# Kernel optimization log

Measured on AMD Instinct MI355X. Metric: run time of the kernel, lower is better.

The kernel has to match this reference:

```python
import jax, jax.numpy as jnp
import numpy as np

B, S, D, H, E, K = 4, 2048, 1024, 2048, 8, 2


def setup_inputs() -> dict:
    key = jax.random.key(0)
    ks = jax.random.split(key, 5)
    x = jax.random.normal(ks[0], (B, S, D), dtype=jnp.float32)
    Wr = jax.random.normal(ks[1], (D, E), dtype=jnp.float32) * 0.02  # router weight
    w1 = jax.random.normal(ks[2], (E, D, H), dtype=jnp.float32) * 0.02  # gate proj per expert
    w3 = jax.random.normal(ks[3], (E, D, H), dtype=jnp.float32) * 0.02  # up proj per expert
    w2 = jax.random.normal(ks[4], (E, H, D), dtype=jnp.float32) * 0.02  # down proj per expert
    return {"x": x, "Wr": Wr, "w1": w1, "w2": w2, "w3": w3}


def reference(x, Wr, w1, w2, w3):
    b, s, d = x.shape
    e = Wr.shape[1]
    flat = x.reshape(b * s, d)                      # [T, D]
    logits = flat @ Wr                              # [T, E]
    probs = jax.nn.softmax(logits, axis=-1)
    vals, idx = jax.lax.top_k(probs, K)             # [T, K]
    weights = vals / jnp.sum(vals, axis=-1, keepdims=True)
    onehot = jax.nn.one_hot(idx, e, dtype=flat.dtype)   # [T, K, E]
    cw = jnp.einsum('tke,tk->te', onehot, weights)      # combine weight per (token, expert)

    # naive dense: every expert computes every token, masked by combine weights
    out = jnp.zeros_like(flat)
    for ei in range(e):  # fixed small structural loop over experts
        h = jax.nn.silu(flat @ w1[ei]) * (flat @ w3[ei])   # [T, H]
        out = out + (h @ w2[ei]) * cw[:, ei:ei + 1]

    # aux load-balancing loss (usage uses any() over top-k slots, as in torch code)
    usage = (onehot.sum(axis=1) > 0).astype(flat.dtype).mean(axis=0)  # [E]
    prob_mass = probs.mean(axis=0)                                     # [E]
    aux_loss = e * jnp.sum(usage * prob_mass)
    return out.reshape(b, s, d), aux_loss
```

## Files before the change

### kernel.cpp

```cpp
#include <hip/hip_runtime.h>
#include <hip/hip_bf16.h>
#include <cstdint>
#include <cstddef>

#define T_TOK 8192
#define DIM   1024
#define HID   2048
#define NE    8
#define CAP   2816

typedef __attribute__((ext_vector_type(8))) short bf16x8;
typedef __attribute__((ext_vector_type(4))) float f32x4;
using bf16 = __hip_bfloat16;

__device__ __forceinline__ void gload16(const bf16* g, bf16* l) {
    __builtin_amdgcn_global_load_lds(
        (const __attribute__((address_space(1))) unsigned int*)(g),
        (__attribute__((address_space(3))) unsigned int*)(l), 16, 0, 0);
}
__device__ __forceinline__ float b2f(unsigned short u) {
    return __uint_as_float(((unsigned int)u) << 16);
}

__global__ void k_convert_x(const float* __restrict__ x, bf16* __restrict__ xb) {
    int i = (blockIdx.x * blockDim.x + threadIdx.x) * 4;
    float4 v = *(const float4*)(x + i);
    bf16 o[4] = {__float2bfloat16(v.x), __float2bfloat16(v.y),
                 __float2bfloat16(v.z), __float2bfloat16(v.w)};
    *(uint2*)(xb + i) = *(const uint2*)o;
}

__global__ __launch_bounds__(256) void k_transpose_bf16(const float* __restrict__ in,
                                                        bf16* __restrict__ out, int R, int C) {
    __shared__ float tile[64][65];
    int e = blockIdx.y;
    int ct = C >> 6;
    int r0 = (blockIdx.x / ct) << 6;
    int c0 = (blockIdx.x % ct) << 6;
    const float* src = in + (size_t)e * R * C;
    bf16* dst = out + (size_t)e * R * C;
    int s = threadIdx.x & 15, g = threadIdx.x >> 4;
#pragma unroll
    for (int j = 0; j < 4; ++j) {
        int row = j * 16 + g;
        float4 v = *(const float4*)(src + (size_t)(r0 + row) * C + c0 + s * 4);
        tile[row][s * 4 + 0] = v.x; tile[row][s * 4 + 1] = v.y;
        tile[row][s * 4 + 2] = v.z; tile[row][s * 4 + 3] = v.w;
    }
    __syncthreads();
#pragma unroll
    for (int j = 0; j < 4; ++j) {
        int c = j * 16 + g;
        int r = s * 4;
        bf16 o[4] = {__float2bfloat16(tile[r][c]),     __float2bfloat16(tile[r + 1][c]),
                     __float2bfloat16(tile[r + 2][c]), __float2bfloat16(tile[r + 3][c])};
        *(uint2*)(dst + (size_t)(c0 + c) * R + r0 + r) = *(const uint2*)o;
    }
}

__global__ __launch_bounds__(256) void k_logits(const float* __restrict__ x,
                                                const float* __restrict__ Wr,
                                                float* __restrict__ logits) {
    __shared__ float wl[NE][DIM];
    for (int o = threadIdx.x; o < NE * DIM; o += 256) {
        int e = o >> 10, d = o & (DIM - 1);
        wl[e][d] = Wr[d * NE + e];
    }
    __syncthreads();
    int wid = threadIdx.x >> 6, lane = threadIdx.x & 63;
    int t = blockIdx.x * 4 + wid;
    const float* xr = x + (size_t)t * DIM;
    double acc[NE];
#pragma unroll
    for (int e = 0; e < NE; ++e) acc[e] = 0.0;
    for (int i = 0; i < DIM / 64; ++i) {
        float xv = xr[i * 64 + lane];
#pragma unroll
        for (int e = 0; e < NE; ++e)
            acc[e] += (double)xv * (double)wl[e][i * 64 + lane];
    }
#pragma unroll
    for (int e = 0; e < NE; ++e) {
        double v = acc[e];
        for (int m = 32; m >= 1; m >>= 1) v += __shfl_xor(v, m);
        if (lane == 0) logits[t * NE + e] = (float)v;
    }
}

__global__ __launch_bounds__(256) void k_route(const float* __restrict__ logits,
                                               int* counts, int* seg_tok, float* seg_w,
                                               int* slotpos, float* probsum) {
    int t = blockIdx.x * 256 + threadIdx.x;
    float l[NE];
#pragma unroll
    for (int e = 0; e < NE; ++e) l[e] = logits[t * NE + e];
    float mx = l[0];
#pragma unroll
    for (int e = 1; e < NE; ++e) mx = fmaxf(mx, l[e]);
    float p[NE], s = 0.f;
#pragma unroll
    for (int e = 0; e < NE; ++e) { p[e] = expf(l[e] - mx); s += p[e]; }
    float inv = 1.f / s;
#pragma unroll
    for (int e = 0; e < NE; ++e) p[e] *= inv;
    int e0 = 0; float v0 = p[0];
#pragma unroll
    for (int e = 1; e < NE; ++e) if (p[e] > v0) { v0 = p[e]; e0 = e; }
    int e1 = -1; float v1 = -1.f;
#pragma unroll
    for (int e = 0; e < NE; ++e) if (e != e0 && p[e] > v1) { v1 = p[e]; e1 = e; }
    float wsum = v0 + v1;
    float w0 = v0 / wsum, w1 = v1 / wsum;

    int lane = threadIdx.x & 63, wid = threadIdx.x >> 6;
    __shared__ float ps[4][NE];
#pragma unroll
    for (int e = 0; e < NE; ++e) {
        float v = p[e];
        for (int m = 32; m >= 1; m >>= 1) v += __shfl_xor(v, m);
        if (lane == 0) ps[wid][e] = v;
    }
    __syncthreads();
    if (threadIdx.x < NE) {
        float v = ps[0][threadIdx.x] + ps[1][threadIdx.x] + ps[2][threadIdx.x] + ps[3][threadIdx.x];
        atomicAdd(&probsum[threadIdx.x], v);
    }
    for (int slot = 0; slot < 2; ++slot) {
        int   e  = slot ? e1 : e0;
        float wv = slot ? w1 : w0;
#pragma unroll
        for (int ex = 0; ex < NE; ++ex) {
            unsigned long long m = __ballot(e == ex);
            if (e == ex) {
                int leader = __ffsll(m) - 1;
                int base = 0;
                if (lane == leader) base = atomicAdd(&counts[ex], __popcll(m));
                base = __shfl(base, leader);
                int pos = base + (int)__popcll(m & ((1ull << lane) - 1ull));
                if (pos < CAP) {
                    seg_tok[ex * CAP + pos] = t;
                    seg_w[ex * CAP + pos]  = wv;
                    slotpos[2 * t + slot]  = ex * CAP + pos;
                } else {
                    slotpos[2 * t + slot]  = -1;
                }
            }
        }
    }
}

__global__ __launch_bounds__(256, 2) void k_gemm1(const bf16* __restrict__ xb,
                                                  const bf16* __restrict__ w1t,
                                                  const bf16* __restrict__ w3t,
                                                  const int* __restrict__ counts,
                                                  const int* __restrict__ seg_tok,
                                                  bf16* __restrict__ h) {
    __shared__ __align__(16) bf16 As[128 * 64];
    __shared__ __align__(16) bf16 Bg[128 * 64];
    __shared__ __align__(16) bf16 Bu[128 * 64];
    __shared__ int toks[128];
    const int NT = HID / 128;
    int flat = blockIdx.y * gridDim.x + blockIdx.x;
    int cpx  = (gridDim.x * NE) >> 3;
    int swz  = (flat & 7) * cpx + (flat >> 3);
    int e    = swz / gridDim.x;
    int tile = swz % gridDim.x;
    int mtile = tile / NT, ntile = tile % NT;
    int cnt = counts[e]; if (cnt > CAP) cnt = CAP;
    if (mtile * 128 >= cnt) return;

    int tx = threadIdx.x;
    if (tx < 128) {
        int slot = mtile * 128 + tx;
        toks[tx] = seg_tok[e * CAP + (slot < cnt ? slot : 0)];
    }
    __syncthreads();

    int lane = tx & 63, w = tx >> 6;
    const bf16 *ap[4], *gp[4], *up[4];
    bf16 *al[4], *gl[4], *ul[4];
#pragma unroll
    for (int i = 0; i < 4; ++i) {
        int seg = w * 4 + i;
        int r = seg * 8 + (lane >> 3);
        int co = (lane & 7) * 8;
        ap[i] = xb  + (size_t)toks[r] * DIM + co;
        gp[i] = w1t + ((size_t)e * HID + ntile * 128 + r) * DIM + co;
        up[i] = w3t + ((size_t)e * HID + ntile * 128 + r) * DIM + co;
        al[i] = As + seg * 512; gl[i] = Bg + seg * 512; ul[i] = Bu + seg * 512;
    }

    f32x4 zero4 = {0.f, 0.f, 0.f, 0.f};
    f32x4 accg[4][4], accu[4][4];
#pragma unroll
    for (int m = 0; m < 4; ++m)
#pragma unroll
        for (int n = 0; n < 4; ++n) { accg[m][n] = zero4; accu[m][n] = zero4; }
    int wr = w >> 1, wc = w & 1;

    for (int k0 = 0; k0 < DIM; k0 += 64) {
#pragma unroll
        for (int i = 0; i < 4; ++i) {
            gload16(ap[i] + k0, al[i]);
            gload16(gp[i] + k0, gl[i]);
            gload16(up[i] + k0, ul[i]);
        }
        __syncthreads();
#pragma unroll
        for (int ks = 0; ks < 2; ++ks) {
            bf16x8 af[4];
#pragma unroll
            for (int m = 0; m < 4; ++m)
                af[m] = *(const bf16x8*)(As + (wr * 64 + m * 16 + (lane & 15)) * 64 + ks * 32 + (lane >> 4) * 8);
#pragma unroll
            for (int n = 0; n < 4; ++n) {
                bf16x8 bgf = *(const bf16x8*)(Bg + (wc * 64 + n * 16 + (lane & 15)) * 64 + ks * 32 + (lane >> 4) * 8);
                bf16x8 buf_ = *(const bf16x8*)(Bu + (wc * 64 + n * 16 + (lane & 15)) * 64 + ks * 32 + (lane >> 4) * 8);
#pragma unroll
                for (int m = 0; m < 4; ++m) {
                    accg[m][n] = __builtin_amdgcn_mfma_f32_16x16x32_bf16(af[m], bgf, accg[m][n], 0, 0, 0);
                    accu[m][n] = __builtin_amdgcn_mfma_f32_16x16x32_bf16(af[m], buf_, accu[m][n], 0, 0, 0);
                }
            }
        }
        __syncthreads();
    }
    bf16* hdst = h + ((size_t)e * CAP + (size_t)mtile * 128) * HID + ntile * 128;
#pragma unroll
    for (int m = 0; m < 4; ++m)
#pragma unroll
        for (int n = 0; n < 4; ++n)
#pragma unroll
            for (int r = 0; r < 4; ++r) {
                int row = wr * 64 + m * 16 + (lane >> 4) * 4 + r;
                int col = wc * 64 + n * 16 + (lane & 15);
                float gg = accg[m][n][r], uu = accu[m][n][r];
                float hv = gg / (1.f + __expf(-gg)) * uu;
                hdst[(size_t)row * HID + col] = __float2bfloat16(hv);
            }
}

__global__ __launch_bounds__(256, 2) void k_gemm2(const bf16* __restrict__ h,
                                                  const bf16* __restrict__ w2t,
                                                  const int* __restrict__ counts,
                                                  const float* __restrict__ seg_w,
                                                  bf16* __restrict__ ybuf) {
    __shared__ __align__(16) bf16 As[128 * 64];
    __shared__ __align__(16) bf16 Bs[128 * 64];
    __shared__ float wts[128];
    const int NT = DIM / 128;
    int flat = blockIdx.y * gridDim.x + blockIdx.x;
    int cpx  = (gridDim.x * NE) >> 3;
    int swz  = (flat & 7) * cpx + (flat >> 3);
    int e    = swz / gridDim.x;
    int tile = swz % gridDim.x;
    int mtile = tile / NT, ntile = tile % NT;
    int cnt = counts[e]; if (cnt > CAP) cnt = CAP;
    if (mtile * 128 >= cnt) return;

    int tx = threadIdx.x;
    if (tx < 128) {
        int slot = mtile * 128 + tx;
        wts[tx] = (slot < cnt) ? seg_w[e * CAP + slot] : 0.f;
    }
    __syncthreads();

    int lane = tx & 63, w = tx >> 6;
    const bf16 *ap[4], *bp[4];
    bf16 *al[4], *bl[4];
#pragma unroll
    for (int i = 0; i < 4; ++i) {
        int seg = w * 4 + i;
        int r = seg * 8 + (lane >> 3);
        int co = (lane & 7) * 8;
        ap[i] = h   + ((size_t)e * CAP + mtile * 128 + r) * HID + co;
        bp[i] = w2t + ((size_t)e * DIM + ntile * 128 + r) * HID + co;
        al[i] = As + seg * 512; bl[i] = Bs + seg * 512;
    }

    f32x4 zero4 = {0.f, 0.f, 0.f, 0.f};
    f32x4 acc[4][4];
#pragma unroll
    for (int m = 0; m < 4; ++m)
#pragma unroll
        for (int n = 0; n < 4; ++n) acc[m][n] = zero4;
    int wr = w >> 1, wc = w & 1;

    for (int k0 = 0; k0 < HID; k0 += 64) {
#pragma unroll
        for (int i = 0; i < 4; ++i) {
            gload16(ap[i] + k0, al[i]);
            gload16(bp[i] + k0, bl[i]);
        }
        __syncthreads();
#pragma unroll
        for (int ks = 0; ks < 2; ++ks) {
            bf16x8 af[4];
#pragma unroll
            for (int m = 0; m < 4; ++m)
                af[m] = *(const bf16x8*)(As + (wr * 64 + m * 16 + (lane & 15)) * 64 + ks * 32 + (lane >> 4) * 8);
#pragma unroll
            for (int n = 0; n < 4; ++n) {
                bf16x8 b = *(const bf16x8*)(Bs + (wc * 64 + n * 16 + (lane & 15)) * 64 + ks * 32 + (lane >> 4) * 8);
#pragma unroll
                for (int m = 0; m < 4; ++m)
                    acc[m][n] = __builtin_amdgcn_mfma_f32_16x16x32_bf16(af[m], b, acc[m][n], 0, 0, 0);
            }
        }
        __syncthreads();
    }
    bf16* ydst = ybuf + ((size_t)e * CAP + (size_t)mtile * 128) * DIM + ntile * 128;
#pragma unroll
    for (int m = 0; m < 4; ++m)
#pragma unroll
        for (int n = 0; n < 4; ++n)
#pragma unroll
            for (int r = 0; r < 4; ++r) {
                int row = wr * 64 + m * 16 + (lane >> 4) * 4 + r;
                int col = wc * 64 + n * 16 + (lane & 15);
                ydst[(size_t)row * DIM + col] = __float2bfloat16(acc[m][n][r] * wts[row]);
            }
}

__global__ __launch_bounds__(256) void k_combine(const bf16* __restrict__ yb,
                                                 const int* __restrict__ slotpos,
                                                 float* __restrict__ out) {
    int t = blockIdx.x;
    int s0 = slotpos[2 * t], s1 = slotpos[2 * t + 1];
    int d = threadIdx.x * 4;
    float4 a = {0.f, 0.f, 0.f, 0.f};
    if (s0 >= 0) {
        ushort4 v = *(const ushort4*)(yb + (size_t)s0 * DIM + d);
        a.x += b2f(v.x); a.y += b2f(v.y); a.z += b2f(v.z); a.w += b2f(v.w);
    }
    if (s1 >= 0) {
        ushort4 v = *(const ushort4*)(yb + (size_t)s1 * DIM + d);
        a.x += b2f(v.x); a.y += b2f(v.y); a.z += b2f(v.z); a.w += b2f(v.w);
    }
    *(float4*)(out + (size_t)t * DIM + d) = a;
}

__global__ void k_aux(const int* __restrict__ counts, const float* __restrict__ probsum,
                      float* __restrict__ outaux) {
    if (threadIdx.x == 0 && blockIdx.x == 0) {
        float s = 0.f;
        for (int e = 0; e < NE; ++e)
            s += ((float)counts[e] / (float)T_TOK) * (probsum[e] / (float)T_TOK);
        *outaux = (float)NE * s;
    }
}

extern "C" void kernel_launch(void* const* d_in, const int* in_sizes, int n_in,
                              void* d_out, int out_size, void* d_ws, size_t ws_size,
                              hipStream_t stream) {
    const float* x  = (const float*)d_in[0];
    const float* Wr = (const float*)d_in[1];
    const float* w1 = (const float*)d_in[2];
    const float* w2 = (const float*)d_in[3];
    const float* w3 = (const float*)d_in[4];
    float* out = (float*)d_out;

    char* ws = (char*)d_ws;
    size_t off = 0;
    auto alloc = [&](size_t bytes) { void* p = ws + off; off += (bytes + 255) & ~(size_t)255; return p; };
    bf16*  xb      = (bf16*)alloc((size_t)T_TOK * DIM * 2);
    bf16*  w1t     = (bf16*)alloc((size_t)NE * HID * DIM * 2);
    bf16*  w3t     = (bf16*)alloc((size_t)NE * HID * DIM * 2);
    bf16*  w2t     = (bf16*)alloc((size_t)NE * DIM * HID * 2);
    bf16*  hbuf    = (bf16*)alloc((size_t)NE * CAP * HID * 2);
    float* logits  = (float*)alloc((size_t)T_TOK * NE * 4);
    int*   counts  = (int*)alloc(256);
    int*   segtok  = (int*)alloc((size_t)NE * CAP * 4);
    float* segw    = (float*)alloc((size_t)NE * CAP * 4);
    int*   slotpos = (int*)alloc((size_t)T_TOK * 2 * 4);
    float* probsum = (float*)alloc(256);
    bf16*  ybuf    = w1t;
    (void)ws_size; (void)in_sizes; (void)n_in;

    hipMemsetAsync(counts, 0, 256, stream);
    hipMemsetAsync(probsum, 0, 256, stream);

    k_convert_x<<<T_TOK * DIM / 4 / 256, 256, 0, stream>>>(x, xb);
    dim3 gt1((DIM / 64) * (HID / 64), NE);
    k_transpose_bf16<<<gt1, 256, 0, stream>>>(w1, w1t, DIM, HID);
    k_transpose_bf16<<<gt1, 256, 0, stream>>>(w3, w3t, DIM, HID);
    dim3 gt2((HID / 64) * (DIM / 64), NE);
    k_transpose_bf16<<<gt2, 256, 0, stream>>>(w2, w2t, HID, DIM);

    k_logits<<<T_TOK / 4, 256, 0, stream>>>(x, Wr, logits);
    k_route<<<T_TOK / 256, 256, 0, stream>>>(logits, counts, segtok, segw, slotpos, probsum);

    dim3 g1((CAP / 128) * (HID / 128), NE);
    k_gemm1<<<g1, 256, 0, stream>>>(xb, w1t, w3t, counts, segtok, hbuf);
    dim3 g2((CAP / 128) * (DIM / 128), NE);
    k_gemm2<<<g2, 256, 0, stream>>>(hbuf, w2t, counts, segw, ybuf);

    k_combine<<<T_TOK, 256, 0, stream>>>(ybuf, slotpos, out);
    k_aux<<<1, 64, 0, stream>>>(counts, probsum, out + (size_t)T_TOK * DIM);
}
```

Before: 439.2 us.

## Double-buffer expert GEMMs with 512-thread blocks and fuse preprocessing launches

Both expert GEMMs are rebuilt around a double-buffered LDS pipeline with a BK=32 k-step, explicit vmcnt waits, XOR-swizzled LDS layouts and 512-thread blocks. In gemm1 the gate and up products are split across warp roles and combined through LDS. gemm2 moves to 256-wide N tiles. The x-to-bf16 conversion is folded into the logits kernel, and the three weight transposes are merged into one launch. The goal is to hide global-load latency behind MFMA work, avoid LDS bank conflicts and cut launch count, at the cost of more barriers per k-step and an extra LDS round trip in the gemm1 epilogue.

```diff
diff --git a/kernel.cpp b/kernel.cpp
--- a/kernel.cpp
+++ b/kernel.cpp
@@ -21,18 +21,23 @@
 __device__ __forceinline__ float b2f(unsigned short u) {
     return __uint_as_float(((unsigned int)u) << 16);
 }
-
-__global__ void k_convert_x(const float* __restrict__ x, bf16* __restrict__ xb) {
-    int i = (blockIdx.x * blockDim.x + threadIdx.x) * 4;
-    float4 v = *(const float4*)(x + i);
-    bf16 o[4] = {__float2bfloat16(v.x), __float2bfloat16(v.y),
-                 __float2bfloat16(v.z), __float2bfloat16(v.w)};
-    *(uint2*)(xb + i) = *(const uint2*)o;
-}
-
-__global__ __launch_bounds__(256) void k_transpose_bf16(const float* __restrict__ in,
-                                                        bf16* __restrict__ out, int R, int C) {
+#define MFMA16(a, b, c) __builtin_amdgcn_mfma_f32_16x16x32_bf16((a), (b), (c), 0, 0, 0)
+#define BARRIER() asm volatile("s_barrier" ::: "memory")
+#define WAITVM3() asm volatile("s_waitcnt vmcnt(3)" ::: "memory")
+#define WAITVM0() asm volatile("s_waitcnt vmcnt(0)" ::: "memory")
+
+__global__ __launch_bounds__(256) void k_transpose_all(const float* __restrict__ w1,
+                                                       const float* __restrict__ w3,
+                                                       const float* __restrict__ w2,
+                                                       bf16* __restrict__ w1t,
+                                                       bf16* __restrict__ w3t,
+                                                       bf16* __restrict__ w2t) {
     __shared__ float tile[64][65];
+    int z = blockIdx.z;
+    const float* in = (z == 0) ? w1 : (z == 1) ? w3 : w2;
+    bf16* out = (z == 0) ? w1t : (z == 1) ? w3t : w2t;
+    int R = (z == 2) ? HID : DIM;
+    int C = (z == 2) ? DIM : HID;
     int e = blockIdx.y;
     int ct = C >> 6;
     int r0 = (blockIdx.x / ct) << 6;
@@ -60,7 +65,8 @@
 
 __global__ __launch_bounds__(256) void k_logits(const float* __restrict__ x,
                                                 const float* __restrict__ Wr,
-                                                float* __restrict__ logits) {
+                                                float* __restrict__ logits,
+                                                bf16* __restrict__ xb) {
     __shared__ float wl[NE][DIM];
     for (int o = threadIdx.x; o < NE * DIM; o += 256) {
         int e = o >> 10, d = o & (DIM - 1);
@@ -73,11 +79,17 @@
     double acc[NE];
 #pragma unroll
     for (int e = 0; e < NE; ++e) acc[e] = 0.0;
-    for (int i = 0; i < DIM / 64; ++i) {
-        float xv = xr[i * 64 + lane];
+#pragma unroll
+    for (int i = 0; i < DIM / 256; ++i) {
+        int base = i * 256 + lane * 4;
+        float4 v = *(const float4*)(xr + base);
+        bf16 o[4] = {__float2bfloat16(v.x), __float2bfloat16(v.y),
+                     __float2bfloat16(v.z), __float2bfloat16(v.w)};
+        *(uint2*)(xb + (size_t)t * DIM + base) = *(const uint2*)o;
 #pragma unroll
         for (int e = 0; e < NE; ++e)
-            acc[e] += (double)xv * (double)wl[e][i * 64 + lane];
+            acc[e] += (double)v.x * wl[e][base] + (double)v.y * wl[e][base + 1]
+                    + (double)v.z * wl[e][base + 2] + (double)v.w * wl[e][base + 3];
     }
 #pragma unroll
     for (int e = 0; e < NE; ++e) {
@@ -149,175 +161,203 @@
     }
 }
 
-__global__ __launch_bounds__(256, 2) void k_gemm1(const bf16* __restrict__ xb,
+__global__ __launch_bounds__(512, 2) void k_gemm1(const bf16* __restrict__ xb,
                                                   const bf16* __restrict__ w1t,
                                                   const bf16* __restrict__ w3t,
                                                   const int* __restrict__ counts,
                                                   const int* __restrict__ seg_tok,
                                                   bf16* __restrict__ h) {
-    __shared__ __align__(16) bf16 As[128 * 64];
-    __shared__ __align__(16) bf16 Bg[128 * 64];
-    __shared__ __align__(16) bf16 Bu[128 * 64];
+    __shared__ __align__(16) bf16 lds[24576];
     __shared__ int toks[128];
-    const int NT = HID / 128;
+    const int NTL = HID / 128;
     int flat = blockIdx.y * gridDim.x + blockIdx.x;
     int cpx  = (gridDim.x * NE) >> 3;
     int swz  = (flat & 7) * cpx + (flat >> 3);
     int e    = swz / gridDim.x;
     int tile = swz % gridDim.x;
-    int mtile = tile / NT, ntile = tile % NT;
+    int mtile = tile / NTL, ntile = tile % NTL;
     int cnt = counts[e]; if (cnt > CAP) cnt = CAP;
     if (mtile * 128 >= cnt) return;
 
-    int tx = threadIdx.x;
+    int tx = threadIdx.x, lane = tx & 63, wid = tx >> 6;
     if (tx < 128) {
         int slot = mtile * 128 + tx;
         toks[tx] = seg_tok[e * CAP + (slot < cnt ? slot : 0)];
     }
     __syncthreads();
 
-    int lane = tx & 63, w = tx >> 6;
-    const bf16 *ap[4], *gp[4], *up[4];
-    bf16 *al[4], *gl[4], *ul[4];
-#pragma unroll
-    for (int i = 0; i < 4; ++i) {
-        int seg = w * 4 + i;
-        int r = seg * 8 + (lane >> 3);
-        int co = (lane & 7) * 8;
-        ap[i] = xb  + (size_t)toks[r] * DIM + co;
-        gp[i] = w1t + ((size_t)e * HID + ntile * 128 + r) * DIM + co;
-        up[i] = w3t + ((size_t)e * HID + ntile * 128 + r) * DIM + co;
-        al[i] = As + seg * 512; gl[i] = Bg + seg * 512; ul[i] = Bu + seg * 512;
-    }
-
+    int srow = tx >> 2;
+    int sc8  = (((tx & 3) ^ ((tx >> 3) & 3)) << 3);
+    const bf16* sA  = xb  + (size_t)toks[srow] * DIM + sc8;
+    const bf16* sBg = w1t + ((size_t)e * HID + ntile * 128 + srow) * DIM + sc8;
+    const bf16* sBu = w3t + ((size_t)e * HID + ntile * 128 + srow) * DIM + sc8;
+
+    int l15 = lane & 15, lh = lane >> 4;
+    int role = wid >> 2, pp = wid & 3, rh = pp >> 1, ch = pp & 1;
+    int ach = ((lh ^ ((l15 >> 1) & 3)) << 3);
+    const int rAoff = (rh * 64 + l15) * 32 + ach;
+    const int rBoff = 4096 + role * 4096 + (ch * 64 + l15) * 32 + ach;
+
+    f32x4 acc[4][4];
     f32x4 zero4 = {0.f, 0.f, 0.f, 0.f};
-    f32x4 accg[4][4], accu[4][4];
 #pragma unroll
     for (int m = 0; m < 4; ++m)
 #pragma unroll
-        for (int n = 0; n < 4; ++n) { accg[m][n] = zero4; accu[m][n] = zero4; }
-    int wr = w >> 1, wc = w & 1;
-
-    for (int k0 = 0; k0 < DIM; k0 += 64) {
-#pragma unroll
-        for (int i = 0; i < 4; ++i) {
-            gload16(ap[i] + k0, al[i]);
-            gload16(gp[i] + k0, gl[i]);
-            gload16(up[i] + k0, ul[i]);
-        }
-        __syncthreads();
-#pragma unroll
-        for (int ks = 0; ks < 2; ++ks) {
-            bf16x8 af[4];
-#pragma unroll
-            for (int m = 0; m < 4; ++m)
-                af[m] = *(const bf16x8*)(As + (wr * 64 + m * 16 + (lane & 15)) * 64 + ks * 32 + (lane >> 4) * 8);
-#pragma unroll
-            for (int n = 0; n < 4; ++n) {
-                bf16x8 bgf = *(const bf16x8*)(Bg + (wc * 64 + n * 16 + (lane & 15)) * 64 + ks * 32 + (lane >> 4) * 8);
-                bf16x8 buf_ = *(const bf16x8*)(Bu + (wc * 64 + n * 16 + (lane & 15)) * 64 + ks * 32 + (lane >> 4) * 8);
-#pragma unroll
-                for (int m = 0; m < 4; ++m) {
-                    accg[m][n] = __builtin_amdgcn_mfma_f32_16x16x32_bf16(af[m], bgf, accg[m][n], 0, 0, 0);
-                    accu[m][n] = __builtin_amdgcn_mfma_f32_16x16x32_bf16(af[m], buf_, accu[m][n], 0, 0, 0);
+        for (int n = 0; n < 4; ++n) acc[m][n] = zero4;
+
+#define G1_STAGE(s, ko) do { \
+        gload16(sA  + (ko), lds + (s) * 12288 + tx * 8); \
+        gload16(sBg + (ko), lds + (s) * 12288 + 4096 + tx * 8); \
+        gload16(sBu + (ko), lds + (s) * 12288 + 8192 + tx * 8); } while (0)
+
+    G1_STAGE(0, 0);
+    const int NT = DIM / 32;
+#pragma unroll 1
+    for (int k = 0; k < NT; ++k) {
+        if (k + 1 < NT) G1_STAGE((k + 1) & 1, (k + 1) * 32);
+        if (k < NT - 1) WAITVM3(); else WAITVM0();
+        BARRIER();
+        const bf16* base = lds + (k & 1) * 12288;
+        bf16x8 a0 = *(const bf16x8*)(base + rAoff);
+        bf16x8 a1 = *(const bf16x8*)(base + rAoff + 512);
+        bf16x8 a2 = *(const bf16x8*)(base + rAoff + 1024);
+        bf16x8 a3 = *(const bf16x8*)(base + rAoff + 1536);
+        bf16x8 b0 = *(const bf16x8*)(base + rBoff);
+        bf16x8 b1 = *(const bf16x8*)(base + rBoff + 512);
+        bf16x8 b2 = *(const bf16x8*)(base + rBoff + 1024);
+        bf16x8 b3 = *(const bf16x8*)(base + rBoff + 1536);
+        __builtin_amdgcn_s_setprio(1);
+        acc[0][0] = MFMA16(a0, b0, acc[0][0]); acc[1][0] = MFMA16(a1, b0, acc[1][0]);
+        acc[2][0] = MFMA16(a2, b0, acc[2][0]); acc[3][0] = MFMA16(a3, b0, acc[3][0]);
+        acc[0][1] = MFMA16(a0, b1, acc[0][1]); acc[1][1] = MFMA16(a1, b1, acc[1][1]);
+        acc[2][1] = MFMA16(a2, b1, acc[2][1]); acc[3][1] = MFMA16(a3, b1, acc[3][1]);
+        acc[0][2] = MFMA16(a0, b2, acc[0][2]); acc[1][2] = MFMA16(a1, b2, acc[1][2]);
+        acc[2][2] = MFMA16(a2, b2, acc[2][2]); acc[3][2] = MFMA16(a3, b2, acc[3][2]);
+        acc[0][3] = MFMA16(a0, b3, acc[0][3]); acc[1][3] = MFMA16(a1, b3, acc[1][3]);
+        acc[2][3] = MFMA16(a2, b3, acc[2][3]); acc[3][3] = MFMA16(a3, b3, acc[3][3]);
+        __builtin_amdgcn_s_setprio(0);
+        BARRIER();
+    }
+#undef G1_STAGE
+
+    if (role == 1) {
+#pragma unroll
+        for (int m = 0; m < 4; ++m)
+#pragma unroll
+            for (int n = 0; n < 4; ++n)
+#pragma unroll
+                for (int r = 0; r < 4; ++r) {
+                    int row = rh * 64 + m * 16 + lh * 4 + r;
+                    int col = ch * 64 + n * 16 + l15;
+                    lds[row * 128 + col] = __float2bfloat16(acc[m][n][r]);
                 }
-            }
-        }
-        __syncthreads();
-    }
-    bf16* hdst = h + ((size_t)e * CAP + (size_t)mtile * 128) * HID + ntile * 128;
-#pragma unroll
-    for (int m = 0; m < 4; ++m)
-#pragma unroll
-        for (int n = 0; n < 4; ++n)
-#pragma unroll
-            for (int r = 0; r < 4; ++r) {
-                int row = wr * 64 + m * 16 + (lane >> 4) * 4 + r;
-                int col = wc * 64 + n * 16 + (lane & 15);
-                float gg = accg[m][n][r], uu = accu[m][n][r];
-                float hv = gg / (1.f + __expf(-gg)) * uu;
-                hdst[(size_t)row * HID + col] = __float2bfloat16(hv);
-            }
-}
-
-__global__ __launch_bounds__(256, 2) void k_gemm2(const bf16* __restrict__ h,
+    }
+    BARRIER();
+    if (role == 0) {
+        bf16* hdst = h + ((size_t)e * CAP + (size_t)mtile * 128) * HID + ntile * 128;
+#pragma unroll
+        for (int m = 0; m < 4; ++m)
+#pragma unroll
+            for (int n = 0; n < 4; ++n)
+#pragma unroll
+                for (int r = 0; r < 4; ++r) {
+                    int row = rh * 64 + m * 16 + lh * 4 + r;
+                    int col = ch * 64 + n * 16 + l15;
+                    float gg = acc[m][n][r];
+                    float uu = b2f(*(const unsigned short*)&lds[row * 128 + col]);
+                    float hv = gg / (1.f + __expf(-gg)) * uu;
+                    hdst[(size_t)row * HID + col] = __float2bfloat16(hv);
+                }
+    }
+}
+
+__global__ __launch_bounds__(512, 2) void k_gemm2(const bf16* __restrict__ hbuf,
                                                   const bf16* __restrict__ w2t,
                                                   const int* __restrict__ counts,
                                                   const float* __restrict__ seg_w,
                                                   bf16* __restrict__ ybuf) {
-    __shared__ __align__(16) bf16 As[128 * 64];
-    __shared__ __align__(16) bf16 Bs[128 * 64];
+    __shared__ __align__(16) bf16 lds[24576];
     __shared__ float wts[128];
-    const int NT = DIM / 128;
+    const int NTL = DIM / 256;
     int flat = blockIdx.y * gridDim.x + blockIdx.x;
     int cpx  = (gridDim.x * NE) >> 3;
     int swz  = (flat & 7) * cpx + (flat >> 3);
     int e    = swz / gridDim.x;
     int tile = swz % gridDim.x;
-    int mtile = tile / NT, ntile = tile % NT;
+    int mtile = tile / NTL, ntile = tile % NTL;
     int cnt = counts[e]; if (cnt > CAP) cnt = CAP;
     if (mtile * 128 >= cnt) return;
 
-    int tx = threadIdx.x;
+    int tx = threadIdx.x, lane = tx & 63, wid = tx >> 6;
     if (tx < 128) {
         int slot = mtile * 128 + tx;
         wts[tx] = (slot < cnt) ? seg_w[e * CAP + slot] : 0.f;
     }
     __syncthreads();
 
-    int lane = tx & 63, w = tx >> 6;
-    const bf16 *ap[4], *bp[4];
-    bf16 *al[4], *bl[4];
-#pragma unroll
-    for (int i = 0; i < 4; ++i) {
-        int seg = w * 4 + i;
-        int r = seg * 8 + (lane >> 3);
-        int co = (lane & 7) * 8;
-        ap[i] = h   + ((size_t)e * CAP + mtile * 128 + r) * HID + co;
-        bp[i] = w2t + ((size_t)e * DIM + ntile * 128 + r) * HID + co;
-        al[i] = As + seg * 512; bl[i] = Bs + seg * 512;
-    }
-
+    int srow = tx >> 2;
+    int sc8  = (((tx & 3) ^ ((tx >> 3) & 3)) << 3);
+    const bf16* sA  = hbuf + ((size_t)e * CAP + mtile * 128 + srow) * HID + sc8;
+    const bf16* sB0 = w2t + ((size_t)e * DIM + ntile * 256 + srow) * HID + sc8;
+    const bf16* sB1 = w2t + ((size_t)e * DIM + ntile * 256 + 128 + srow) * HID + sc8;
+
+    int l15 = lane & 15, lh = lane >> 4;
+    int rh = wid >> 2, cq = wid & 3;
+    int ach = ((lh ^ ((l15 >> 1) & 3)) << 3);
+    const int rAoff = (rh * 64 + l15) * 32 + ach;
+    const int rBoff = 4096 + (cq * 64 + l15) * 32 + ach;
+
+    f32x4 acc[4][4];
     f32x4 zero4 = {0.f, 0.f, 0.f, 0.f};
-    f32x4 acc[4][4];
 #pragma unroll
     for (int m = 0; m < 4; ++m)
 #pragma unroll
         for (int n = 0; n < 4; ++n) acc[m][n] = zero4;
-    int wr = w >> 1, wc = w & 1;
-
-    for (int k0 = 0; k0 < HID; k0 += 64) {
-#pragma unroll
-        for (int i = 0; i < 4; ++i) {
-            gload16(ap[i] + k0, al[i]);
-            gload16(bp[i] + k0, bl[i]);
-        }
-        __syncthreads();
-#pragma unroll
-        for (int ks = 0; ks < 2; ++ks) {
-            bf16x8 af[4];
-#pragma unroll
-            for (int m = 0; m < 4; ++m)
-                af[m] = *(const bf16x8*)(As + (wr * 64 + m * 16 + (lane & 15)) * 64 + ks * 32 + (lane >> 4) * 8);
-#pragma unroll
-            for (int n = 0; n < 4; ++n) {
-                bf16x8 b = *(const bf16x8*)(Bs + (wc * 64 + n * 16 + (lane & 15)) * 64 + ks * 32 + (lane >> 4) * 8);
-#pragma unroll
-                for (int m = 0; m < 4; ++m)
-                    acc[m][n] = __builtin_amdgcn_mfma_f32_16x16x32_bf16(af[m], b, acc[m][n], 0, 0, 0);
-            }
-        }
-        __syncthreads();
-    }
-    bf16* ydst = ybuf + ((size_t)e * CAP + (size_t)mtile * 128) * DIM + ntile * 128;
+
+#define G2_STAGE(s, ko) do { \
+        gload16(sA  + (ko), lds + (s) * 12288 + tx * 8); \
+        gload16(sB0 + (ko), lds + (s) * 12288 + 4096 + tx * 8); \
+        gload16(sB1 + (ko), lds + (s) * 12288 + 8192 + tx * 8); } while (0)
+
+    G2_STAGE(0, 0);
+    const int NT = HID / 32;
+#pragma unroll 1
+    for (int k = 0; k < NT; ++k) {
+        if (k + 1 < NT) G2_STAGE((k + 1) & 1, (k + 1) * 32);
+        if (k < NT - 1) WAITVM3(); else WAITVM0();
+        BARRIER();
+        const bf16* base = lds + (k & 1) * 12288;
+        bf16x8 a0 = *(const bf16x8*)(base + rAoff);
+        bf16x8 a1 = *(const bf16x8*)(base + rAoff + 512);
+        bf16x8 a2 = *(const bf16x8*)(base + rAoff + 1024);
+        bf16x8 a3 = *(const bf16x8*)(base + rAoff + 1536);
+        bf16x8 b0 = *(const bf16x8*)(base + rBoff);
+        bf16x8 b1 = *(const bf16x8*)(base + rBoff + 512);
+        bf16x8 b2 = *(const bf16x8*)(base + rBoff + 1024);
+        bf16x8 b3 = *(const bf16x8*)(base + rBoff + 1536);
+        __builtin_amdgcn_s_setprio(1);
+        acc[0][0] = MFMA16(a0, b0, acc[0][0]); acc[1][0] = MFMA16(a1, b0, acc[1][0]);
+        acc[2][0] = MFMA16(a2, b0, acc[2][0]); acc[3][0] = MFMA16(a3, b0, acc[3][0]);
+        acc[0][1] = MFMA16(a0, b1, acc[0][1]); acc[1][1] = MFMA16(a1, b1, acc[1][1]);
+        acc[2][1] = MFMA16(a2, b1, acc[2][1]); acc[3][1] = MFMA16(a3, b1, acc[3][1]);
+        acc[0][2] = MFMA16(a0, b2, acc[0][2]); acc[1][2] = MFMA16(a1, b2, acc[1][2]);
+        acc[2][2] = MFMA16(a2, b2, acc[2][2]); acc[3][2] = MFMA16(a3, b2, acc[3][2]);
+        acc[0][3] = MFMA16(a0, b3, acc[0][3]); acc[1][3] = MFMA16(a1, b3, acc[1][3]);
+        acc[2][3] = MFMA16(a2, b3, acc[2][3]); acc[3][3] = MFMA16(a3, b3, acc[3][3]);
+        __builtin_amdgcn_s_setprio(0);
+        BARRIER();
+    }
+#undef G2_STAGE
+
+    bf16* ydst = ybuf + ((size_t)e * CAP + (size_t)mtile * 128) * DIM + ntile * 256;
 #pragma unroll
     for (int m = 0; m < 4; ++m)
 #pragma unroll
         for (int n = 0; n < 4; ++n)
 #pragma unroll
             for (int r = 0; r < 4; ++r) {
-                int row = wr * 64 + m * 16 + (lane >> 4) * 4 + r;
-                int col = wc * 64 + n * 16 + (lane & 15);
+                int row = rh * 64 + m * 16 + lh * 4 + r;
+                int col = cq * 64 + n * 16 + l15;
                 ydst[(size_t)row * DIM + col] = __float2bfloat16(acc[m][n][r] * wts[row]);
             }
 }
@@ -380,20 +420,16 @@
     hipMemsetAsync(counts, 0, 256, stream);
     hipMemsetAsync(probsum, 0, 256, stream);
 
-    k_convert_x<<<T_TOK * DIM / 4 / 256, 256, 0, stream>>>(x, xb);
-    dim3 gt1((DIM / 64) * (HID / 64), NE);
-    k_transpose_bf16<<<gt1, 256, 0, stream>>>(w1, w1t, DIM, HID);
-    k_transpose_bf16<<<gt1, 256, 0, stream>>>(w3, w3t, DIM, HID);
-    dim3 gt2((HID / 64) * (DIM / 64), NE);
-    k_transpose_bf16<<<gt2, 256, 0, stream>>>(w2, w2t, HID, DIM);
-
-    k_logits<<<T_TOK / 4, 256, 0, stream>>>(x, Wr, logits);
+    k_logits<<<T_TOK / 4, 256, 0, stream>>>(x, Wr, logits, xb);
     k_route<<<T_TOK / 256, 256, 0, stream>>>(logits, counts, segtok, segw, slotpos, probsum);
 
+    dim3 gt((DIM / 64) * (HID / 64), NE, 3);
+    k_transpose_all<<<gt, 256, 0, stream>>>(w1, w3, w2, w1t, w3t, w2t);
+
     dim3 g1((CAP / 128) * (HID / 128), NE);
-    k_gemm1<<<g1, 256, 0, stream>>>(xb, w1t, w3t, counts, segtok, hbuf);
-    dim3 g2((CAP / 128) * (DIM / 128), NE);
-    k_gemm2<<<g2, 256, 0, stream>>>(hbuf, w2t, counts, segw, ybuf);
+    k_gemm1<<<g1, 512, 0, stream>>>(xb, w1t, w3t, counts, segtok, hbuf);
+    dim3 g2((CAP / 128) * (DIM / 256), NE);
+    k_gemm2<<<g2, 512, 0, stream>>>(hbuf, w2t, counts, segw, ybuf);
 
     k_combine<<<T_TOK, 256, 0, stream>>>(ybuf, slotpos, out);
     k_aux<<<1, 64, 0, stream>>>(counts, probsum, out + (size_t)T_TOK * DIM);
```

New measurement: 427.6 us. 2.6% less time.

## Fuse x conversion into logits, merge transposes, swizzle LDS, shrink gemm1 tile

Applied to the files above, without the earlier changes.

The standalone x-to-bf16 conversion kernel is folded into the logits kernel, which now reads x as float4. The three weight transposes become one launch using blockIdx.z. Both expert GEMMs gain an XOR-swizzled LDS layout to cut bank conflicts. gemm1 drops to a 128x64 N-tile with a smaller accumulator set and occupancy hint 3, trading more blocks and more A reloads for lower register pressure.

```diff
diff --git a/kernel.cpp b/kernel.cpp
--- a/kernel.cpp
+++ b/kernel.cpp
@@ -21,18 +21,20 @@
 __device__ __forceinline__ float b2f(unsigned short u) {
     return __uint_as_float(((unsigned int)u) << 16);
 }
-
-__global__ void k_convert_x(const float* __restrict__ x, bf16* __restrict__ xb) {
-    int i = (blockIdx.x * blockDim.x + threadIdx.x) * 4;
-    float4 v = *(const float4*)(x + i);
-    bf16 o[4] = {__float2bfloat16(v.x), __float2bfloat16(v.y),
-                 __float2bfloat16(v.z), __float2bfloat16(v.w)};
-    *(uint2*)(xb + i) = *(const uint2*)o;
-}
-
-__global__ __launch_bounds__(256) void k_transpose_bf16(const float* __restrict__ in,
-                                                        bf16* __restrict__ out, int R, int C) {
+#define MFMA16(a, b, c) __builtin_amdgcn_mfma_f32_16x16x32_bf16((a), (b), (c), 0, 0, 0)
+
+__global__ __launch_bounds__(256) void k_transpose_all(const float* __restrict__ w1,
+                                                       const float* __restrict__ w3,
+                                                       const float* __restrict__ w2,
+                                                       bf16* __restrict__ w1t,
+                                                       bf16* __restrict__ w3t,
+                                                       bf16* __restrict__ w2t) {
     __shared__ float tile[64][65];
+    int z = blockIdx.z;
+    const float* in = (z == 0) ? w1 : (z == 1) ? w3 : w2;
+    bf16* out = (z == 0) ? w1t : (z == 1) ? w3t : w2t;
+    int R = (z == 2) ? HID : DIM;
+    int C = (z == 2) ? DIM : HID;
     int e = blockIdx.y;
     int ct = C >> 6;
     int r0 = (blockIdx.x / ct) << 6;
@@ -60,7 +62,8 @@
 
 __global__ __launch_bounds__(256) void k_logits(const float* __restrict__ x,
                                                 const float* __restrict__ Wr,
-                                                float* __restrict__ logits) {
+                                                float* __restrict__ logits,
+                                                bf16* __restrict__ xb) {
     __shared__ float wl[NE][DIM];
     for (int o = threadIdx.x; o < NE * DIM; o += 256) {
         int e = o >> 10, d = o & (DIM - 1);
@@ -73,11 +76,17 @@
     double acc[NE];
 #pragma unroll
     for (int e = 0; e < NE; ++e) acc[e] = 0.0;
-    for (int i = 0; i < DIM / 64; ++i) {
-        float xv = xr[i * 64 + lane];
+#pragma unroll
+    for (int i = 0; i < DIM / 256; ++i) {
+        int base = i * 256 + lane * 4;
+        float4 v = *(const float4*)(xr + base);
+        bf16 o[4] = {__float2bfloat16(v.x), __float2bfloat16(v.y),
+                     __float2bfloat16(v.z), __float2bfloat16(v.w)};
+        *(uint2*)(xb + (size_t)t * DIM + base) = *(const uint2*)o;
 #pragma unroll
         for (int e = 0; e < NE; ++e)
-            acc[e] += (double)xv * (double)wl[e][i * 64 + lane];
+            acc[e] += (double)v.x * wl[e][base] + (double)v.y * wl[e][base + 1]
+                    + (double)v.z * wl[e][base + 2] + (double)v.w * wl[e][base + 3];
     }
 #pragma unroll
     for (int e = 0; e < NE; ++e) {
@@ -149,166 +158,186 @@
     }
 }
 
-__global__ __launch_bounds__(256, 2) void k_gemm1(const bf16* __restrict__ xb,
+__global__ __launch_bounds__(256, 3) void k_gemm1(const bf16* __restrict__ xb,
                                                   const bf16* __restrict__ w1t,
                                                   const bf16* __restrict__ w3t,
                                                   const int* __restrict__ counts,
                                                   const int* __restrict__ seg_tok,
                                                   bf16* __restrict__ h) {
-    __shared__ __align__(16) bf16 As[128 * 64];
-    __shared__ __align__(16) bf16 Bg[128 * 64];
-    __shared__ __align__(16) bf16 Bu[128 * 64];
+    __shared__ __align__(16) bf16 lds[16384];
     __shared__ int toks[128];
-    const int NT = HID / 128;
+    const int NTL = HID / 64;
     int flat = blockIdx.y * gridDim.x + blockIdx.x;
     int cpx  = (gridDim.x * NE) >> 3;
     int swz  = (flat & 7) * cpx + (flat >> 3);
     int e    = swz / gridDim.x;
     int tile = swz % gridDim.x;
-    int mtile = tile / NT, ntile = tile % NT;
+    int mtile = tile / NTL, ntile = tile % NTL;
     int cnt = counts[e]; if (cnt > CAP) cnt = CAP;
     if (mtile * 128 >= cnt) return;
 
-    int tx = threadIdx.x;
+    int tx = threadIdx.x, lane = tx & 63, w = tx >> 6;
     if (tx < 128) {
         int slot = mtile * 128 + tx;
         toks[tx] = seg_tok[e * CAP + (slot < cnt ? slot : 0)];
     }
     __syncthreads();
 
-    int lane = tx & 63, w = tx >> 6;
-    const bf16 *ap[4], *gp[4], *up[4];
-    bf16 *al[4], *gl[4], *ul[4];
-#pragma unroll
-    for (int i = 0; i < 4; ++i) {
-        int seg = w * 4 + i;
-        int r = seg * 8 + (lane >> 3);
-        int co = (lane & 7) * 8;
-        ap[i] = xb  + (size_t)toks[r] * DIM + co;
-        gp[i] = w1t + ((size_t)e * HID + ntile * 128 + r) * DIM + co;
-        up[i] = w3t + ((size_t)e * HID + ntile * 128 + r) * DIM + co;
-        al[i] = As + seg * 512; gl[i] = Bg + seg * 512; ul[i] = Bu + seg * 512;
-    }
-
+    int l8 = lane >> 3;
+    int sch = (((lane & 7) ^ l8) << 3);
+    const bf16* sA[4];
+#pragma unroll
+    for (int i = 0; i < 4; ++i)
+        sA[i] = xb + (size_t)toks[w * 32 + i * 8 + l8] * DIM + sch;
+    const bf16* sBg[2];
+    const bf16* sBu[2];
+#pragma unroll
+    for (int j = 0; j < 2; ++j) {
+        int br = ntile * 64 + w * 16 + j * 8 + l8;
+        sBg[j] = w1t + ((size_t)e * HID + br) * DIM + sch;
+        sBu[j] = w3t + ((size_t)e * HID + br) * DIM + sch;
+    }
+    bf16* dA  = lds + w * 2048 + (lane << 3);
+    bf16* dBg = lds + 8192  + w * 1024 + (lane << 3);
+    bf16* dBu = lds + 12288 + w * 1024 + (lane << 3);
+
+    int l15 = lane & 15, lh = lane >> 4;
+    int wm = w >> 1, wn = w & 1;
+    f32x4 accg[4][2], accu[4][2];
     f32x4 zero4 = {0.f, 0.f, 0.f, 0.f};
-    f32x4 accg[4][4], accu[4][4];
 #pragma unroll
     for (int m = 0; m < 4; ++m)
 #pragma unroll
-        for (int n = 0; n < 4; ++n) { accg[m][n] = zero4; accu[m][n] = zero4; }
-    int wr = w >> 1, wc = w & 1;
-
-    for (int k0 = 0; k0 < DIM; k0 += 64) {
-#pragma unroll
-        for (int i = 0; i < 4; ++i) {
-            gload16(ap[i] + k0, al[i]);
-            gload16(gp[i] + k0, gl[i]);
-            gload16(up[i] + k0, ul[i]);
+        for (int n = 0; n < 2; ++n) { accg[m][n] = zero4; accu[m][n] = zero4; }
+
+    const int NT = DIM / 64;
+#pragma unroll 1
+    for (int k = 0; k < NT; ++k) {
+        int ko = k * 64;
+#pragma unroll
+        for (int i = 0; i < 4; ++i) gload16(sA[i] + ko, dA + i * 512);
+#pragma unroll
+        for (int j = 0; j < 2; ++j) {
+            gload16(sBg[j] + ko, dBg + j * 512);
+            gload16(sBu[j] + ko, dBu + j * 512);
         }
         __syncthreads();
 #pragma unroll
         for (int ks = 0; ks < 2; ++ks) {
-            bf16x8 af[4];
-#pragma unroll
-            for (int m = 0; m < 4; ++m)
-                af[m] = *(const bf16x8*)(As + (wr * 64 + m * 16 + (lane & 15)) * 64 + ks * 32 + (lane >> 4) * 8);
-#pragma unroll
-            for (int n = 0; n < 4; ++n) {
-                bf16x8 bgf = *(const bf16x8*)(Bg + (wc * 64 + n * 16 + (lane & 15)) * 64 + ks * 32 + (lane >> 4) * 8);
-                bf16x8 buf_ = *(const bf16x8*)(Bu + (wc * 64 + n * 16 + (lane & 15)) * 64 + ks * 32 + (lane >> 4) * 8);
+            int co = ((((ks << 2) | lh) ^ (l15 & 7)) << 3);
+            bf16x8 af[4], bg[2], bu[2];
+#pragma unroll
+            for (int m = 0; m < 4; ++m) {
+                int row = wm * 64 + m * 16 + l15;
+                af[m] = *(const bf16x8*)(lds + row * 64 + co);
+            }
+#pragma unroll
+            for (int n = 0; n < 2; ++n) {
+                int br = wn * 32 + n * 16 + l15;
+                bg[n] = *(const bf16x8*)(lds + 8192 + br * 64 + co);
+                bu[n] = *(const bf16x8*)(lds + 12288 + br * 64 + co);
+            }
+#pragma unroll
+            for (int n = 0; n < 2; ++n)
 #pragma unroll
                 for (int m = 0; m < 4; ++m) {
-                    accg[m][n] = __builtin_amdgcn_mfma_f32_16x16x32_bf16(af[m], bgf, accg[m][n], 0, 0, 0);
-                    accu[m][n] = __builtin_amdgcn_mfma_f32_16x16x32_bf16(af[m], buf_, accu[m][n], 0, 0, 0);
+                    accg[m][n] = MFMA16(af[m], bg[n], accg[m][n]);
+                    accu[m][n] = MFMA16(af[m], bu[n], accu[m][n]);
                 }
-            }
         }
         __syncthreads();
     }
-    bf16* hdst = h + ((size_t)e * CAP + (size_t)mtile * 128) * HID + ntile * 128;
+
+    bf16* hdst = h + ((size_t)e * CAP + (size_t)mtile * 128) * HID + ntile * 64;
 #pragma unroll
     for (int m = 0; m < 4; ++m)
 #pragma unroll
-        for (int n = 0; n < 4; ++n)
+        for (int n = 0; n < 2; ++n)
 #pragma unroll
             for (int r = 0; r < 4; ++r) {
-                int row = wr * 64 + m * 16 + (lane >> 4) * 4 + r;
-                int col = wc * 64 + n * 16 + (lane & 15);
+                int row = wm * 64 + m * 16 + lh * 4 + r;
+                int col = wn * 32 + n * 16 + l15;
                 float gg = accg[m][n][r], uu = accu[m][n][r];
                 float hv = gg / (1.f + __expf(-gg)) * uu;
                 hdst[(size_t)row * HID + col] = __float2bfloat16(hv);
             }
 }
 
-__global__ __launch_bounds__(256, 2) void k_gemm2(const bf16* __restrict__ h,
+__global__ __launch_bounds__(256, 3) void k_gemm2(const bf16* __restrict__ hbuf,
                                                   const bf16* __restrict__ w2t,
                                                   const int* __restrict__ counts,
                                                   const float* __restrict__ seg_w,
                                                   bf16* __restrict__ ybuf) {
-    __shared__ __align__(16) bf16 As[128 * 64];
-    __shared__ __align__(16) bf16 Bs[128 * 64];
+    __shared__ __align__(16) bf16 lds[16384];
     __shared__ float wts[128];
-    const int NT = DIM / 128;
+    const int NTL = DIM / 128;
     int flat = blockIdx.y * gridDim.x + blockIdx.x;
     int cpx  = (gridDim.x * NE) >> 3;
     int swz  = (flat & 7) * cpx + (flat >> 3);
     int e    = swz / gridDim.x;
     int tile = swz % gridDim.x;
-    int mtile = tile / NT, ntile = tile % NT;
+    int mtile = tile / NTL, ntile = tile % NTL;
     int cnt = counts[e]; if (cnt > CAP) cnt = CAP;
     if (mtile * 128 >= cnt) return;
 
-    int tx = threadIdx.x;
+    int tx = threadIdx.x, lane = tx & 63, w = tx >> 6;
     if (tx < 128) {
         int slot = mtile * 128 + tx;
         wts[tx] = (slot < cnt) ? seg_w[e * CAP + slot] : 0.f;
     }
     __syncthreads();
 
-    int lane = tx & 63, w = tx >> 6;
-    const bf16 *ap[4], *bp[4];
-    bf16 *al[4], *bl[4];
+    int l8 = lane >> 3;
+    int sch = (((lane & 7) ^ l8) << 3);
+    const bf16* sA[4];
+    const bf16* sB[4];
 #pragma unroll
     for (int i = 0; i < 4; ++i) {
-        int seg = w * 4 + i;
-        int r = seg * 8 + (lane >> 3);
-        int co = (lane & 7) * 8;
-        ap[i] = h   + ((size_t)e * CAP + mtile * 128 + r) * HID + co;
-        bp[i] = w2t + ((size_t)e * DIM + ntile * 128 + r) * HID + co;
-        al[i] = As + seg * 512; bl[i] = Bs + seg * 512;
-    }
-
+        sA[i] = hbuf + ((size_t)e * CAP + mtile * 128 + w * 32 + i * 8 + l8) * HID + sch;
+        sB[i] = w2t + ((size_t)e * DIM + ntile * 128 + w * 32 + i * 8 + l8) * HID + sch;
+    }
+    bf16* dA = lds + w * 2048 + (lane << 3);
+    bf16* dB = lds + 8192 + w * 2048 + (lane << 3);
+
+    int l15 = lane & 15, lh = lane >> 4;
+    int wm = w >> 1, wn = w & 1;
+    f32x4 acc[4][4];
     f32x4 zero4 = {0.f, 0.f, 0.f, 0.f};
-    f32x4 acc[4][4];
 #pragma unroll
     for (int m = 0; m < 4; ++m)
 #pragma unroll
         for (int n = 0; n < 4; ++n) acc[m][n] = zero4;
-    int wr = w >> 1, wc = w & 1;
-
-    for (int k0 = 0; k0 < HID; k0 += 64) {
+
+    const int NT = HID / 64;
+#pragma unroll 1
+    for (int k = 0; k < NT; ++k) {
+        int ko = k * 64;
 #pragma unroll
         for (int i = 0; i < 4; ++i) {
-            gload16(ap[i] + k0, al[i]);
-            gload16(bp[i] + k0, bl[i]);
+            gload16(sA[i] + ko, dA + i * 512);
+            gload16(sB[i] + ko, dB + i * 512);
         }
         __syncthreads();
 #pragma unroll
         for (int ks = 0; ks < 2; ++ks) {
-            bf16x8 af[4];
-#pragma unroll
-            for (int m = 0; m < 4; ++m)
-                af[m] = *(const bf16x8*)(As + (wr * 64 + m * 16 + (lane & 15)) * 64 + ks * 32 + (lane >> 4) * 8);
-#pragma unroll
-            for (int n = 0; n < 4; ++n) {
-                bf16x8 b = *(const bf16x8*)(Bs + (wc * 64 + n * 16 + (lane & 15)) * 64 + ks * 32 + (lane >> 4) * 8);
+            int co = ((((ks << 2) | lh) ^ (l15 & 7)) << 3);
+            bf16x8 af[4], bf_[4];
+#pragma unroll
+            for (int m = 0; m < 4; ++m) {
+                int row = wm * 64 + m * 16 + l15;
+                af[m] = *(const bf16x8*)(lds + row * 64 + co);
+                int br = wn * 64 + m * 16 + l15;
+                bf_[m] = *(const bf16x8*)(lds + 8192 + br * 64 + co);
+            }
+#pragma unroll
+            for (int n = 0; n < 4; ++n)
 #pragma unroll
                 for (int m = 0; m < 4; ++m)
-                    acc[m][n] = __builtin_amdgcn_mfma_f32_16x16x32_bf16(af[m], b, acc[m][n], 0, 0, 0);
-            }
+                    acc[m][n] = MFMA16(af[m], bf_[n], acc[m][n]);
         }
         __syncthreads();
     }
+
     bf16* ydst = ybuf + ((size_t)e * CAP + (size_t)mtile * 128) * DIM + ntile * 128;
 #pragma unroll
     for (int m = 0; m < 4; ++m)
@@ -316,8 +345,8 @@
         for (int n = 0; n < 4; ++n)
 #pragma unroll
             for (int r = 0; r < 4; ++r) {
-                int row = wr * 64 + m * 16 + (lane >> 4) * 4 + r;
-                int col = wc * 64 + n * 16 + (lane & 15);
+                int row = wm * 64 + m * 16 + lh * 4 + r;
+                int col = wn * 64 + n * 16 + l15;
                 ydst[(size_t)row * DIM + col] = __float2bfloat16(acc[m][n][r] * wts[row]);
             }
 }
@@ -380,17 +409,13 @@
     hipMemsetAsync(counts, 0, 256, stream);
     hipMemsetAsync(probsum, 0, 256, stream);
 
-    k_convert_x<<<T_TOK * DIM / 4 / 256, 256, 0, stream>>>(x, xb);
-    dim3 gt1((DIM / 64) * (HID / 64), NE);
-    k_transpose_bf16<<<gt1, 256, 0, stream>>>(w1, w1t, DIM, HID);
-    k_transpose_bf16<<<gt1, 256, 0, stream>>>(w3, w3t, DIM, HID);
-    dim3 gt2((HID / 64) * (DIM / 64), NE);
-    k_transpose_bf16<<<gt2, 256, 0, stream>>>(w2, w2t, HID, DIM);
-
-    k_logits<<<T_TOK / 4, 256, 0, stream>>>(x, Wr, logits);
+    k_logits<<<T_TOK / 4, 256, 0, stream>>>(x, Wr, logits, xb);
     k_route<<<T_TOK / 256, 256, 0, stream>>>(logits, counts, segtok, segw, slotpos, probsum);
 
-    dim3 g1((CAP / 128) * (HID / 128), NE);
+    dim3 gt((DIM / 64) * (HID / 64), NE, 3);
+    k_transpose_all<<<gt, 256, 0, stream>>>(w1, w3, w2, w1t, w3t, w2t);
+
+    dim3 g1((CAP / 128) * (HID / 64), NE);
     k_gemm1<<<g1, 256, 0, stream>>>(xb, w1t, w3t, counts, segtok, hbuf);
     dim3 g2((CAP / 128) * (DIM / 128), NE);
     k_gemm2<<<g2, 256, 0, stream>>>(hbuf, w2t, counts, segw, ybuf);
```

Measured after the change: 387.6 us. -11.7%, faster.
